# Performance work log

Hardware: AMD Instinct MI355X
Metric: run time of the kernel (lower is better)

The kernel has to match this reference:

```python
import jax, jax.numpy as jnp
import numpy as np

N, C, T, V, O, S, R = 32, 64, 256, 25, 192, 3, 8  # batch, in_ch, time, joints, out_ch, subsets, rel_ch


def setup_inputs() -> dict:
    key = jax.random.key(0)
    ks = jax.random.split(key, 20)
    w = lambda i, shape: (jax.random.normal(ks[i], shape, jnp.float32) * 0.05)
    return {
        "x": jax.random.normal(ks[0], (N, C, T, V), jnp.float32),
        "spd_A": jax.random.normal(ks[1], (V, V), jnp.float32) * 0.1,
        "A3": jax.random.normal(ks[2], (S, V, V), jnp.float32) * 0.1,
        "A6": jax.random.normal(ks[3], (6, V, V), jnp.float32) * 0.1,
        "conv1_w": w(4, (S, R, C)), "conv1_b": jnp.zeros((S, R), jnp.float32),
        "conv2_w": w(5, (S, R, C)), "conv2_b": jnp.zeros((S, R), jnp.float32),
        "conv4_w": w(6, (S, O, R)), "conv4_b": jnp.zeros((S, O), jnp.float32),
        "conv3_w": w(7, (S, O, C)), "conv3_b": jnp.zeros((S, O), jnp.float32),
        "alpha": jnp.full((1,), 0.5, jnp.float32),
        "beta": jnp.full((1,), 0.5, jnp.float32),
        "gamma": jnp.full((1,), 0.5, jnp.float32),
        "bn_w": jnp.ones((O,), jnp.float32), "bn_b": jnp.zeros((O,), jnp.float32),
        "down_w": w(8, (O, C)), "down_b": jnp.zeros((O,), jnp.float32),
        "dbn_w": jnp.ones((O,), jnp.float32), "dbn_b": jnp.zeros((O,), jnp.float32),
    }


def _bn(y, w, b):
    # BatchNorm2d in training mode: stats over (N, T, V) per channel, biased var
    mu = y.mean(axis=(0, 2, 3), keepdims=True)
    var = ((y - mu) ** 2).mean(axis=(0, 2, 3), keepdims=True)
    return (y - mu) * jax.lax.rsqrt(var + 1e-5) * w[None, :, None, None] + b[None, :, None, None]


def reference(x, spd_A, A3, A6, conv1_w, conv1_b, conv2_w, conv2_b, conv4_w, conv4_b,
              conv3_w, conv3_b, alpha, beta, gamma, bn_w, bn_b, down_w, down_b, dbn_w, dbn_b):
    out_c = conv4_w.shape[1]
    # A6 expanded: (out//6, 6, V, V) -> (out, V, V); contiguous-view == tile along channel blocks
    A6_ex = jnp.tile(A6, (out_c // 6, 1, 1))  # (O, V, V)
    # 1x1 conv then temporal mean == conv on temporal mean (linear op commutes)
    xm = x.mean(axis=2)  # (N, C, V)
    x1 = jnp.einsum('ncv,src->nsrv', xm, conv1_w) + conv1_b[None, :, :, None]
    x2 = jnp.einsum('ncv,src->nsrv', xm, conv2_w) + conv2_b[None, :, :, None]
    d = jnp.tanh(x1[..., :, None] - x2[..., None, :])  # (N, S, R, V, V)
    A_dyn = jnp.einsum('nsruv,sor->nsouv', d, conv4_w) + conv4_b[None, :, :, None, None]
    A_at = (A_dyn * alpha + A3[None, :, None, :, :]
            + A6_ex[None, None] * beta + spd_A[None, None, None] * gamma)  # (N, S, O, V, V)
    # CTRGC_2: x3 = conv3(x); einsum 'ncuv,nctv->nctu', summed over subsets
    x3 = jnp.einsum('nctv,soc->nsotv', x, conv3_w) + conv3_b[None, :, :, None, None]
    y = jnp.einsum('nsouv,nsotv->notu', A_at, x3)  # (N, O, T, V)
    y = _bn(y, bn_w, bn_b)
    xd = jnp.einsum('nctv,oc->notv', x, down_w) + down_b[None, :, None, None]
    y = jax.nn.relu(y + _bn(xd, dbn_w, dbn_b))
    return y
```

## Files before the change

kernel.cpp:

```cpp
#include <hip/hip_runtime.h>

#define N_ 32
#define C_ 64
#define T_ 256
#define V_ 25
#define O_ 192
#define S_ 3
#define R_ 8
#define VV (V_*V_)
#define TV (T_*V_)
#define RP 26
#define TRP (T_*RP)

typedef unsigned short u16;
typedef unsigned int u32;
typedef __attribute__((ext_vector_type(4))) u16 u16x4;
typedef __attribute__((ext_vector_type(8))) u16 u16x8;
typedef __attribute__((ext_vector_type(4))) u32 u32x4;
typedef __attribute__((ext_vector_type(8))) __bf16 bf16x8;
typedef __attribute__((ext_vector_type(4))) float f32x4;

#define WS_A2F_U 0
#define WS_XQ_U  (18874368)
#define WS_XD_U  (18874368 + 13631488)
#define WS_YB_U  (18874368 + 13631488 + 39321600)
#define WS_XM_F   (55574528)
#define WS_RS_F   (55574528 + 51200)
#define WS_STAT_F (55574528 + 51200 + 153600)

__device__ __forceinline__ u16 f2b(float f) {
    return __builtin_bit_cast(u16, (__bf16)f);
}
__device__ __forceinline__ float b2f(u16 u) {
    return __builtin_bit_cast(float, ((unsigned)u) << 16);
}
__device__ __forceinline__ f32x4 mfma16(bf16x8 a, bf16x8 b, f32x4 c) {
    return __builtin_amdgcn_mfma_f32_16x16x32_bf16(a, b, c, 0, 0, 0);
}
__device__ __forceinline__ float fast_tanh(float x) {
    return 1.f - 2.f * __builtin_amdgcn_rcpf(__expf(2.f * x) + 1.f);
}

__global__ void k0_xq(const float* __restrict__ x, u16* __restrict__ xq) {
    __shared__ float tile[64][52];
    int bid = blockIdx.x;
    int n = bid >> 7, tb = bid & 127;
    int t0 = tb * 2;
    int tid = threadIdx.x;
    const float2* xp = (const float2*)(x + (size_t)n * C_ * TV + t0 * 25);
    for (int p = tid; p < 1600; p += 256) {
        int c = p / 25, q = p % 25;
        float2 f2 = xp[(size_t)c * 3200 + q];
        tile[c][q * 2] = f2.x;
        tile[c][q * 2 + 1] = f2.y;
    }
    __syncthreads();
    for (int p = tid; p < 832; p += 256) {
        int row = p >> 4, c4g = p & 15;
        int t = row >= RP, v = row - t * RP;
        u16x4 w;
        #pragma unroll
        for (int i = 0; i < 4; ++i) {
            int co = ((c4g & 3) << 4) + ((c4g >> 2) << 2) + i;
            w[i] = (v < 25) ? f2b(tile[co][t * 25 + v]) : (u16)0;
        }
        *(u16x4*)&xq[((size_t)n * TRP + tb * 52 + row) * 64 + c4g * 4] = w;
    }
}

__global__ void k1_xm(const u16* __restrict__ xq, float* __restrict__ xm_out) {
    __shared__ float ps[256];
    int bid = blockIdx.x;
    int n = bid / 25, v = bid % 25;
    int tid = threadIdx.x;
    int cg = tid & 63, tg = tid >> 6;
    const u16* p = xq + (size_t)n * TRP * 64 + ((size_t)(tg * 64 * RP + v)) * 64 + cg;
    float s = 0.f;
    for (int t = 0; t < 64; ++t) {
        s += b2f(*p);
        p += RP * 64;
    }
    ps[tid] = s;
    __syncthreads();
    if (tid < 64) {
        float tot = ps[tid] + ps[64 + tid] + ps[128 + tid] + ps[192 + tid];
        int c4g = tid >> 2, i = tid & 3;
        int co = ((c4g & 3) << 4) + ((c4g >> 2) << 2) + i;
        xm_out[((size_t)n * C_ + co) * V_ + v] = tot * (1.f / T_);
    }
}

__global__ void k2_a2f(const float* __restrict__ spd, const float* __restrict__ A3,
                       const float* __restrict__ A6,
                       const float* __restrict__ w1, const float* __restrict__ b1,
                       const float* __restrict__ w2, const float* __restrict__ b2,
                       const float* __restrict__ w4, const float* __restrict__ b4,
                       const float* __restrict__ b3,
                       const float* __restrict__ alpha, const float* __restrict__ beta,
                       const float* __restrict__ gamma,
                       u16* __restrict__ a2f, const float* __restrict__ xmbuf,
                       float* __restrict__ rs_tot) {
    __shared__ float xm[C_ * V_];
    __shared__ float x1s[R_ * V_], x2s[R_ * V_];
    __shared__ float dm[R_ * VV];
    __shared__ float a3s[VV], sps[VV];
    __shared__ float aatw[4][2 * VV];
    int bid = blockIdx.x;
    int n = bid / 24;
    int rem = bid % 24;
    int s = rem / 8, og = rem % 8;
    int tid = threadIdx.x, wid = tid >> 6, lane = tid & 63;
    const float* xmg = xmbuf + (size_t)n * C_ * V_;
    for (int p = tid; p < C_ * V_; p += 256) xm[p] = xmg[p];
    for (int p = tid; p < VV; p += 256) { a3s[p] = A3[s * VV + p]; sps[p] = spd[p]; }
    __syncthreads();
    if (tid < R_ * V_) {
        int r = tid / V_, v = tid % V_;
        float acc1 = b1[s * R_ + r], acc2 = b2[s * R_ + r];
        for (int c = 0; c < C_; ++c) {
            float xv = xm[c * V_ + v];
            acc1 += xv * w1[(s * R_ + r) * C_ + c];
            acc2 += xv * w2[(s * R_ + r) * C_ + c];
        }
        x1s[tid] = acc1; x2s[tid] = acc2;
    }
    __syncthreads();
    for (int p = tid; p < R_ * VV; p += 256) {
        int r = p / VV, uv = p % VV, u = uv / V_, v = uv % V_;
        dm[p] = fast_tanh(x1s[r * V_ + u] - x2s[r * V_ + v]);
    }
    __syncthreads();
    float al = alpha[0], be = beta[0], ga = gamma[0];
    float* aat = aatw[wid];
    for (int opi = 0; opi < 3; ++opi) {
        int op = wid * 3 + opi;
        int o0 = og * 24 + op * 2;
        float w4v[2][R_], b4v[2];
        #pragma unroll
        for (int oo = 0; oo < 2; ++oo) {
            b4v[oo] = b4[s * O_ + o0 + oo];
            #pragma unroll
            for (int r = 0; r < R_; ++r)
                w4v[oo][r] = w4[((size_t)(s * O_ + o0 + oo)) * R_ + r];
        }
        const float* a6p0 = A6 + ((o0 % 6) * VV);
        for (int p = lane; p < 2 * VV; p += 64) {
            int oo = p / VV, pp = p - oo * VV;
            float acc = b4v[oo];
            #pragma unroll
            for (int r = 0; r < R_; ++r) acc += dm[r * VV + pp] * w4v[oo][r];
            aat[p] = al * acc + a3s[pp] + ga * sps[pp] + be * a6p0[oo * VV + pp];
        }
        if (lane < 2 * V_) {
            int oo = lane / V_, u = lane - oo * V_;
            float rs = 0.f;
            for (int v = 0; v < V_; ++v) rs += aat[oo * VV + u * V_ + v];
            atomicAdd(&rs_tot[((size_t)(n * O_ + o0 + oo)) * V_ + u],
                      b3[s * O_ + o0 + oo] * rs);
        }
        #pragma unroll
        for (int it = 0; it < 4; ++it) {
            int idx = it * 64 + lane;
            int oo = idx >> 7, l2 = idx & 127, cu = l2 >> 6, l = l2 & 63;
            int u = cu * 16 + (l & 15);
            u16x8 w;
            #pragma unroll
            for (int j = 0; j < 8; ++j) {
                int v = ((j >> 2) << 4) + ((l >> 4) << 2) + (j & 3);
                float val = 0.f;
                if (u < V_ && v < V_) val = aat[oo * VV + u * V_ + v];
                w[j] = f2b(val);
            }
            size_t idxg = ((((size_t)(n * O_ + o0 + oo)) * S_ + s) * 2 + cu) * 64 + l;
            ((u16x8*)a2f)[idxg] = w;
        }
    }
}

#define OSTR_B 2504
#define SSTR_B 832
#define BUF_B  20064

__global__ __launch_bounds__(256, 3)
void k3_main(const u16* __restrict__ xq,
             const float* __restrict__ w3, const float* __restrict__ dw,
             const float* __restrict__ db,
             const u16* __restrict__ a2f, const float* __restrict__ rs_tot,
             u16* __restrict__ yb16, u16* __restrict__ xdws,
             float* __restrict__ stats) {
    __shared__ char x3Lb[2 * BUF_B];
    __shared__ u16 xdst[8 * 416];
    __shared__ u16 ystage[8 * 400];
    int orig = blockIdx.x;
    int bid = (orig & 7) * 96 + (orig >> 3);
    int n = bid / 24;
    int o0 = (bid % 24) * 8;
    int tid = threadIdx.x, wid = tid >> 6, lane = tid & 63;
    int lr = lane & 15, lg = lane >> 4;
    int colt = wid & 1;
    int rt0 = (wid >> 1) * 13;

    for (int p = tid; p < 2 * BUF_B / 16; p += 256) ((u32x4*)x3Lb)[p] = u32x4{0,0,0,0};

    const float* wsrc = (colt == 0)
        ? w3 + ((size_t)((lr >> 3) * O_ + o0 + (lr & 7))) * C_
        : ((lr < 8) ? w3 + ((size_t)(2 * O_ + o0 + lr)) * C_
                    : dw + ((size_t)(o0 + lr - 8)) * C_);
    bf16x8 bw[2];
    #pragma unroll
    for (int ks = 0; ks < 2; ++ks) {
        u16x8 tmp;
        #pragma unroll
        for (int j = 0; j < 8; ++j) {
            int c = ks * 32 + (lg << 2) + (j & 3) + ((j >> 2) << 4);
            tmp[j] = f2b(wsrc[c]);
        }
        bw[ks] = __builtin_bit_cast(bf16x8, tmp);
    }
    float dbv = (colt == 1 && lr >= 8) ? db[o0 + lr - 8] : 0.f;

    int wo = (colt == 0) ? (lr & 7) : lr;
    int wsb = (colt == 0) ? (lr >> 3) : 2;
    int colbyte = wo * OSTR_B + wsb * SSTR_B;

    const bf16x8* a2v = (const bf16x8*)a2f;
    bf16x8 Bh[2][6];
    float rsb0[2], rsb1[2];
    #pragma unroll
    for (int oi = 0; oi < 2; ++oi) {
        int o = o0 + (wid << 1) + oi;
        const bf16x8* bp = a2v + ((size_t)(n * O_ + o)) * 6 * 64 + lane;
        #pragma unroll
        for (int q = 0; q < 6; ++q) Bh[oi][q] = bp[(size_t)q * 64];
        const float* rsp = rs_tot + ((size_t)(n * O_ + o)) * V_;
        rsb0[oi] = rsp[lr];
        rsb1[oi] = (lr < 9) ? rsp[16 + lr] : 0.f;
    }

    float sy1[2] = {0, 0}, sy2[2] = {0, 0};
    float sd1 = 0.f, sd2 = 0.f;
    const u16* xbn = xq + (size_t)n * TRP * 64;
    int rdw = 13 * lr + 2 * lg;
    char* buf = x3Lb;
    int t0 = 0;

    auto tl = [&](int ch, int j, u16x8& A0, u16x8& A1) {
        const u16* p = xbn + ((size_t)(ch * 16) * RP + (size_t)((rt0 + j) * 16 + lr)) * 64
                       + (lg << 4);
        A0 = *(const u16x8*)p;
        A1 = *(const u16x8*)(p + 8);
    };
    auto proc = [&](int rt, u16x8 A0, u16x8 A1) {
        f32x4 acc = {0.f, 0.f, 0.f, 0.f};
        acc = mfma16(__builtin_bit_cast(bf16x8, A0), bw[0], acc);
        acc = mfma16(__builtin_bit_cast(bf16x8, A1), bw[1], acc);
        int rbase = rt * 16 + (lg << 2);
        if (colt == 0 || lr < 8) {
            u16x4 w;
            #pragma unroll
            for (int reg = 0; reg < 4; ++reg) w[reg] = f2b(acc[reg]);
            *(u16x4*)(buf + colbyte + rbase * 2) = w;
        } else {
            u16x4 w;
            #pragma unroll
            for (int reg = 0; reg < 4; ++reg) {
                int rr = rbase + reg;
                int t = rr / RP, v = rr - t * RP;
                float val = acc[reg] + dbv;
                w[reg] = f2b(val);
                if (v < 25) { sd1 += val; sd2 += val * val; }
            }
            *(u16x4*)&xdst[(lr - 8) * 416 + rbase] = w;
        }
    };

    __syncthreads();

    u16x8 p0a, p0b, p1a, p1b, p2a, p2b, p3a, p3b;
    tl(0, 0, p0a, p0b); tl(0, 1, p1a, p1b); tl(0, 2, p2a, p2b); tl(0, 3, p3a, p3b);

    for (int ch = 0; ch < 16; ++ch) {
        t0 = ch * 16;
        buf = x3Lb + (ch & 1) * BUF_B;
        proc(rt0 + 0, p0a, p0b);
        proc(rt0 + 1, p1a, p1b);
        proc(rt0 + 2, p2a, p2b);
        proc(rt0 + 3, p3a, p3b);
        for (int j = 4; j < 13; ++j) {
            u16x8 A0, A1;
            tl(ch, j, A0, A1);
            proc(rt0 + j, A0, A1);
        }
        if (ch < 15) {
            tl(ch + 1, 0, p0a, p0b); tl(ch + 1, 1, p1a, p1b);
            tl(ch + 1, 2, p2a, p2b); tl(ch + 1, 3, p3a, p3b);
        }
        __syncthreads();
        #pragma unroll
        for (int oi = 0; oi < 2; ++oi) {
            int ol = (wid << 1) + oi;
            const u32* L = (const u32*)(buf + ol * OSTR_B);
            f32x4 acc0 = {0, 0, 0, 0}, acc1 = {0, 0, 0, 0};
            #pragma unroll
            for (int s = 0; s < 3; ++s) {
                const u32* Ls = L + s * 208 + rdw;
                u32 d0 = Ls[0], d1 = Ls[1], d8 = Ls[8], d9 = Ls[9];
                bf16x8 A = __builtin_bit_cast(bf16x8, u32x4{d0, d1, d8, d9});
                acc0 = mfma16(A, Bh[oi][s * 2 + 0], acc0);
                acc1 = mfma16(A, Bh[oi][s * 2 + 1], acc1);
            }
            int ylb = ol * 400 + (lg << 2) * 25;
            #pragma unroll
            for (int reg = 0; reg < 4; ++reg) {
                float v0 = acc0[reg] + rsb0[oi];
                ystage[ylb + reg * 25 + lr] = f2b(v0);
                sy1[oi] += v0; sy2[oi] += v0 * v0;
                if (lr < 9) {
                    float v1 = acc1[reg] + rsb1[oi];
                    ystage[ylb + reg * 25 + 16 + lr] = f2b(v1);
                    sy1[oi] += v1; sy2[oi] += v1 * v1;
                }
            }
        }
        {
            size_t ygb = (size_t)(n * O_ + o0) * TV + (size_t)t0 * V_;
            for (int q = lane; q < 100; q += 64) {
                int sel = q >= 50;
                int ol2 = (wid << 1) + sel;
                int j = q - sel * 50;
                u16x8 pk = *(const u16x8*)&ystage[ol2 * 400 + j * 8];
                *(u16x8*)&yb16[ygb + (size_t)ol2 * TV + j * 8] = pk;
            }
        }
        if (colt == 1) {
            int tofs = (wid >> 1) * 8;
            size_t gdb = (size_t)(n * O_ + o0) * TV + (size_t)(t0 + tofs) * V_;
            for (int q = lane; q < 200; q += 64) {
                int o = q / 25, w = q - o * 25;
                int g0 = w * 8;
                int tl2 = g0 / 25, v = g0 - tl2 * 25;
                u16x8 pk;
                #pragma unroll
                for (int k = 0; k < 8; ++k) {
                    pk[k] = xdst[o * 416 + (tofs + tl2) * RP + v];
                    if (++v == 25) { v = 0; ++tl2; }
                }
                *(u16x8*)&xdws[gdb + (size_t)o * TV + g0] = pk;
            }
        }
    }
    #pragma unroll
    for (int oi = 0; oi < 2; ++oi) {
        float v1 = sy1[oi], v2 = sy2[oi];
        #pragma unroll
        for (int m = 1; m < 64; m <<= 1) {
            v1 += __shfl_xor(v1, m);
            v2 += __shfl_xor(v2, m);
        }
        if (lane == 0) {
            atomicAdd(&stats[0 * O_ + o0 + (wid << 1) + oi], v1);
            atomicAdd(&stats[1 * O_ + o0 + (wid << 1) + oi], v2);
        }
    }
    if (colt == 1) {
        float v1 = sd1, v2 = sd2;
        v1 += __shfl_xor(v1, 16); v2 += __shfl_xor(v2, 16);
        v1 += __shfl_xor(v1, 32); v2 += __shfl_xor(v2, 32);
        if (lane >= 8 && lane < 16) {
            atomicAdd(&stats[2 * O_ + o0 + lane - 8], v1);
            atomicAdd(&stats[3 * O_ + o0 + lane - 8], v2);
        }
    }
}

__global__ void k5_final(float* __restrict__ out, const u16* __restrict__ yb,
                         const u16* __restrict__ xd, const float* __restrict__ stats,
                         const float* __restrict__ bn_w, const float* __restrict__ bn_b,
                         const float* __restrict__ dbn_w, const float* __restrict__ dbn_b) {
    __shared__ float cf[4 * O_];
    int tid = threadIdx.x;
    if (tid < O_) {
        int o = tid;
        float inv = 1.f / (float)(N_ * T_ * V_);
        float mu_y = stats[o] * inv;
        float var_y = stats[O_ + o] * inv - mu_y * mu_y;
        float ay = bn_w[o] * rsqrtf(var_y + 1e-5f);
        float by = bn_b[o] - mu_y * ay;
        float mu_d = stats[2 * O_ + o] * inv;
        float var_d = stats[3 * O_ + o] * inv - mu_d * mu_d;
        float ad = dbn_w[o] * rsqrtf(var_d + 1e-5f);
        float bd = dbn_b[o] - mu_d * ad;
        cf[o] = ay; cf[O_ + o] = by; cf[2 * O_ + o] = ad; cf[3 * O_ + o] = bd;
    }
    __syncthreads();
    size_t total = (size_t)N_ * O_ * TV / 8;
    for (size_t i = blockIdx.x * (size_t)blockDim.x + tid; i < total;
         i += (size_t)gridDim.x * blockDim.x) {
        int o = (int)((i / 800) % O_);
        float ay = cf[o], by = cf[O_ + o], ad = cf[2 * O_ + o], bd = cf[3 * O_ + o];
        u16x8 yv = ((const u16x8*)yb)[i];
        u16x8 dv = ((const u16x8*)xd)[i];
        float4 r0, r1;
        r0.x = fmaxf(ay * b2f(yv[0]) + by + ad * b2f(dv[0]) + bd, 0.f);
        r0.y = fmaxf(ay * b2f(yv[1]) + by + ad * b2f(dv[1]) + bd, 0.f);
        r0.z = fmaxf(ay * b2f(yv[2]) + by + ad * b2f(dv[2]) + bd, 0.f);
        r0.w = fmaxf(ay * b2f(yv[3]) + by + ad * b2f(dv[3]) + bd, 0.f);
        r1.x = fmaxf(ay * b2f(yv[4]) + by + ad * b2f(dv[4]) + bd, 0.f);
        r1.y = fmaxf(ay * b2f(yv[5]) + by + ad * b2f(dv[5]) + bd, 0.f);
        r1.z = fmaxf(ay * b2f(yv[6]) + by + ad * b2f(dv[6]) + bd, 0.f);
        r1.w = fmaxf(ay * b2f(yv[7]) + by + ad * b2f(dv[7]) + bd, 0.f);
        ((float4*)out)[2 * i] = r0;
        ((float4*)out)[2 * i + 1] = r1;
    }
}

extern "C" void kernel_launch(void* const* d_in, const int* in_sizes, int n_in,
                              void* d_out, int out_size, void* d_ws, size_t ws_size,
                              hipStream_t stream) {
    const float* x     = (const float*)d_in[0];
    const float* spd   = (const float*)d_in[1];
    const float* A3    = (const float*)d_in[2];
    const float* A6    = (const float*)d_in[3];
    const float* w1    = (const float*)d_in[4];
    const float* b1    = (const float*)d_in[5];
    const float* w2    = (const float*)d_in[6];
    const float* b2    = (const float*)d_in[7];
    const float* w4    = (const float*)d_in[8];
    const float* b4    = (const float*)d_in[9];
    const float* w3    = (const float*)d_in[10];
    const float* b3    = (const float*)d_in[11];
    const float* alpha = (const float*)d_in[12];
    const float* beta  = (const float*)d_in[13];
    const float* gamma = (const float*)d_in[14];
    const float* bn_w  = (const float*)d_in[15];
    const float* bn_b  = (const float*)d_in[16];
    const float* dw    = (const float*)d_in[17];
    const float* db    = (const float*)d_in[18];
    const float* dbn_w = (const float*)d_in[19];
    const float* dbn_b = (const float*)d_in[20];
    float* out = (float*)d_out;
    u16*   wsu = (u16*)d_ws;
    float* wsf = (float*)d_ws;

    u16* a2f  = wsu + WS_A2F_U;
    u16* xq   = wsu + WS_XQ_U;
    u16* xd   = wsu + WS_XD_U;
    u16* yb   = wsu + WS_YB_U;
    float* xm    = wsf + WS_XM_F;
    float* rs    = wsf + WS_RS_F;
    float* stats = wsf + WS_STAT_F;

    hipMemsetAsync(rs, 0, (N_ * O_ * V_ + 4 * O_) * sizeof(float), stream);

    k0_xq<<<N_ * 128, 256, 0, stream>>>(x, xq);
    k1_xm<<<N_ * 25, 256, 0, stream>>>(xq, xm);
    k2_a2f<<<N_ * S_ * 8, 256, 0, stream>>>(spd, A3, A6, w1, b1, w2, b2, w4, b4, b3,
                                            alpha, beta, gamma, a2f, xm, rs);
    k3_main<<<N_ * 24, 256, 0, stream>>>(xq, w3, dw, db, a2f, rs, yb, xd, stats);
    k5_final<<<4096, 256, 0, stream>>>(out, yb, xd, stats, bn_w, bn_b, dbn_w, dbn_b);
}
```

Before: 308.7 us.

## Double k3_main block to 512 threads, one output channel per wave

k3_main now launches 512 threads (8 waves) per block instead of 256. Each wave handles one output channel rather than two, and the 26 row tiles of the x3 conv are split 7/7/6/6 across the four wave pairs. The register prefetch pipeline of the next chunk's inputs is removed and replaced by straightforward loads. A second barrier per chunk is added, and every wave now writes its own xd rows. The intent is more parallelism and latency hiding per block, at the cost of lost software prefetch and extra synchronisation.

```diff
diff --git a/kernel.cpp b/kernel.cpp
--- a/kernel.cpp
+++ b/kernel.cpp
@@ -181,7 +181,7 @@
 #define SSTR_B 832
 #define BUF_B  20064
 
-__global__ __launch_bounds__(256, 3)
+__global__ __launch_bounds__(512, 6)
 void k3_main(const u16* __restrict__ xq,
              const float* __restrict__ w3, const float* __restrict__ dw,
              const float* __restrict__ db,
@@ -198,9 +198,11 @@
     int tid = threadIdx.x, wid = tid >> 6, lane = tid & 63;
     int lr = lane & 15, lg = lane >> 4;
     int colt = wid & 1;
-    int rt0 = (wid >> 1) * 13;
-
-    for (int p = tid; p < 2 * BUF_B / 16; p += 256) ((u32x4*)x3Lb)[p] = u32x4{0,0,0,0};
+    int tq = wid >> 1;
+    int rt0 = tq * 7 - (tq == 3 ? 1 : 0);
+    int cnt = (tq < 2) ? 7 : 6;
+
+    for (int p = tid; p < 2 * BUF_B / 16; p += 512) ((u32x4*)x3Lb)[p] = u32x4{0,0,0,0};
 
     const float* wsrc = (colt == 0)
         ? w3 + ((size_t)((lr >> 3) * O_ + o0 + (lr & 7))) * C_
@@ -224,142 +226,114 @@
     int colbyte = wo * OSTR_B + wsb * SSTR_B;
 
     const bf16x8* a2v = (const bf16x8*)a2f;
-    bf16x8 Bh[2][6];
-    float rsb0[2], rsb1[2];
-    #pragma unroll
-    for (int oi = 0; oi < 2; ++oi) {
-        int o = o0 + (wid << 1) + oi;
+    bf16x8 Bh[6];
+    float rsb0, rsb1;
+    {
+        int o = o0 + wid;
         const bf16x8* bp = a2v + ((size_t)(n * O_ + o)) * 6 * 64 + lane;
         #pragma unroll
-        for (int q = 0; q < 6; ++q) Bh[oi][q] = bp[(size_t)q * 64];
+        for (int q = 0; q < 6; ++q) Bh[q] = bp[(size_t)q * 64];
         const float* rsp = rs_tot + ((size_t)(n * O_ + o)) * V_;
-        rsb0[oi] = rsp[lr];
-        rsb1[oi] = (lr < 9) ? rsp[16 + lr] : 0.f;
-    }
-
-    float sy1[2] = {0, 0}, sy2[2] = {0, 0};
+        rsb0 = rsp[lr];
+        rsb1 = (lr < 9) ? rsp[16 + lr] : 0.f;
+    }
+
+    float sy1 = 0.f, sy2 = 0.f;
     float sd1 = 0.f, sd2 = 0.f;
     const u16* xbn = xq + (size_t)n * TRP * 64;
     int rdw = 13 * lr + 2 * lg;
-    char* buf = x3Lb;
-    int t0 = 0;
-
-    auto tl = [&](int ch, int j, u16x8& A0, u16x8& A1) {
-        const u16* p = xbn + ((size_t)(ch * 16) * RP + (size_t)((rt0 + j) * 16 + lr)) * 64
-                       + (lg << 4);
-        A0 = *(const u16x8*)p;
-        A1 = *(const u16x8*)(p + 8);
-    };
-    auto proc = [&](int rt, u16x8 A0, u16x8 A1) {
-        f32x4 acc = {0.f, 0.f, 0.f, 0.f};
-        acc = mfma16(__builtin_bit_cast(bf16x8, A0), bw[0], acc);
-        acc = mfma16(__builtin_bit_cast(bf16x8, A1), bw[1], acc);
-        int rbase = rt * 16 + (lg << 2);
-        if (colt == 0 || lr < 8) {
-            u16x4 w;
-            #pragma unroll
-            for (int reg = 0; reg < 4; ++reg) w[reg] = f2b(acc[reg]);
-            *(u16x4*)(buf + colbyte + rbase * 2) = w;
-        } else {
-            u16x4 w;
-            #pragma unroll
-            for (int reg = 0; reg < 4; ++reg) {
-                int rr = rbase + reg;
-                int t = rr / RP, v = rr - t * RP;
-                float val = acc[reg] + dbv;
-                w[reg] = f2b(val);
-                if (v < 25) { sd1 += val; sd2 += val * val; }
-            }
-            *(u16x4*)&xdst[(lr - 8) * 416 + rbase] = w;
-        }
-    };
-
-    __syncthreads();
-
-    u16x8 p0a, p0b, p1a, p1b, p2a, p2b, p3a, p3b;
-    tl(0, 0, p0a, p0b); tl(0, 1, p1a, p1b); tl(0, 2, p2a, p2b); tl(0, 3, p3a, p3b);
+
+    __syncthreads();
 
     for (int ch = 0; ch < 16; ++ch) {
-        t0 = ch * 16;
-        buf = x3Lb + (ch & 1) * BUF_B;
-        proc(rt0 + 0, p0a, p0b);
-        proc(rt0 + 1, p1a, p1b);
-        proc(rt0 + 2, p2a, p2b);
-        proc(rt0 + 3, p3a, p3b);
-        for (int j = 4; j < 13; ++j) {
-            u16x8 A0, A1;
-            tl(ch, j, A0, A1);
-            proc(rt0 + j, A0, A1);
-        }
-        if (ch < 15) {
-            tl(ch + 1, 0, p0a, p0b); tl(ch + 1, 1, p1a, p1b);
-            tl(ch + 1, 2, p2a, p2b); tl(ch + 1, 3, p3a, p3b);
+        int t0 = ch * 16;
+        char* buf = x3Lb + (ch & 1) * BUF_B;
+        const u16* xrow = xbn + (size_t)t0 * RP * 64;
+        for (int j = 0; j < cnt; ++j) {
+            int rt = rt0 + j;
+            const u16* ap = xrow + (size_t)(rt * 16 + lr) * 64 + (lg << 4);
+            u16x8 A0 = *(const u16x8*)ap;
+            u16x8 A1 = *(const u16x8*)(ap + 8);
+            f32x4 acc = {0.f, 0.f, 0.f, 0.f};
+            acc = mfma16(__builtin_bit_cast(bf16x8, A0), bw[0], acc);
+            acc = mfma16(__builtin_bit_cast(bf16x8, A1), bw[1], acc);
+            int rbase = rt * 16 + (lg << 2);
+            if (colt == 0 || lr < 8) {
+                u16x4 w;
+                #pragma unroll
+                for (int reg = 0; reg < 4; ++reg) w[reg] = f2b(acc[reg]);
+                *(u16x4*)(buf + colbyte + rbase * 2) = w;
+            } else {
+                u16x4 w;
+                #pragma unroll
+                for (int reg = 0; reg < 4; ++reg) {
+                    int rr = rbase + reg;
+                    int t = rr / RP, v = rr - t * RP;
+                    float val = acc[reg] + dbv;
+                    w[reg] = f2b(val);
+                    if (v < 25) { sd1 += val; sd2 += val * val; }
+                }
+                *(u16x4*)&xdst[(lr - 8) * 416 + rbase] = w;
+            }
         }
         __syncthreads();
-        #pragma unroll
-        for (int oi = 0; oi < 2; ++oi) {
-            int ol = (wid << 1) + oi;
-            const u32* L = (const u32*)(buf + ol * OSTR_B);
+        {
+            const u32* L = (const u32*)(buf + wid * OSTR_B);
             f32x4 acc0 = {0, 0, 0, 0}, acc1 = {0, 0, 0, 0};
             #pragma unroll
             for (int s = 0; s < 3; ++s) {
                 const u32* Ls = L + s * 208 + rdw;
                 u32 d0 = Ls[0], d1 = Ls[1], d8 = Ls[8], d9 = Ls[9];
                 bf16x8 A = __builtin_bit_cast(bf16x8, u32x4{d0, d1, d8, d9});
-                acc0 = mfma16(A, Bh[oi][s * 2 + 0], acc0);
-                acc1 = mfma16(A, Bh[oi][s * 2 + 1], acc1);
-            }
-            int ylb = ol * 400 + (lg << 2) * 25;
+                acc0 = mfma16(A, Bh[s * 2 + 0], acc0);
+                acc1 = mfma16(A, Bh[s * 2 + 1], acc1);
+            }
+            int ylb = wid * 400 + (lg << 2) * 25;
             #pragma unroll
             for (int reg = 0; reg < 4; ++reg) {
-                float v0 = acc0[reg] + rsb0[oi];
+                float v0 = acc0[reg] + rsb0;
                 ystage[ylb + reg * 25 + lr] = f2b(v0);
-                sy1[oi] += v0; sy2[oi] += v0 * v0;
+                sy1 += v0; sy2 += v0 * v0;
                 if (lr < 9) {
-                    float v1 = acc1[reg] + rsb1[oi];
+                    float v1 = acc1[reg] + rsb1;
                     ystage[ylb + reg * 25 + 16 + lr] = f2b(v1);
-                    sy1[oi] += v1; sy2[oi] += v1 * v1;
+                    sy1 += v1; sy2 += v1 * v1;
                 }
             }
         }
         {
-            size_t ygb = (size_t)(n * O_ + o0) * TV + (size_t)t0 * V_;
-            for (int q = lane; q < 100; q += 64) {
-                int sel = q >= 50;
-                int ol2 = (wid << 1) + sel;
-                int j = q - sel * 50;
-                u16x8 pk = *(const u16x8*)&ystage[ol2 * 400 + j * 8];
-                *(u16x8*)&yb16[ygb + (size_t)ol2 * TV + j * 8] = pk;
-            }
-        }
-        if (colt == 1) {
-            int tofs = (wid >> 1) * 8;
-            size_t gdb = (size_t)(n * O_ + o0) * TV + (size_t)(t0 + tofs) * V_;
-            for (int q = lane; q < 200; q += 64) {
-                int o = q / 25, w = q - o * 25;
-                int g0 = w * 8;
+            size_t ygb = (size_t)(n * O_ + o0 + wid) * TV + (size_t)t0 * V_;
+            if (lane < 50) {
+                u16x8 pk = *(const u16x8*)&ystage[wid * 400 + lane * 8];
+                *(u16x8*)&yb16[ygb + lane * 8] = pk;
+            }
+        }
+        {
+            size_t gdb = (size_t)(n * O_ + o0 + wid) * TV + (size_t)t0 * V_;
+            if (lane < 50) {
+                int g0 = lane * 8;
                 int tl2 = g0 / 25, v = g0 - tl2 * 25;
                 u16x8 pk;
                 #pragma unroll
                 for (int k = 0; k < 8; ++k) {
-                    pk[k] = xdst[o * 416 + (tofs + tl2) * RP + v];
+                    pk[k] = xdst[wid * 416 + tl2 * RP + v];
                     if (++v == 25) { v = 0; ++tl2; }
                 }
-                *(u16x8*)&xdws[gdb + (size_t)o * TV + g0] = pk;
-            }
-        }
-    }
-    #pragma unroll
-    for (int oi = 0; oi < 2; ++oi) {
-        float v1 = sy1[oi], v2 = sy2[oi];
+                *(u16x8*)&xdws[gdb + g0] = pk;
+            }
+        }
+        __syncthreads();
+    }
+    {
+        float v1 = sy1, v2 = sy2;
         #pragma unroll
         for (int m = 1; m < 64; m <<= 1) {
             v1 += __shfl_xor(v1, m);
             v2 += __shfl_xor(v2, m);
         }
         if (lane == 0) {
-            atomicAdd(&stats[0 * O_ + o0 + (wid << 1) + oi], v1);
-            atomicAdd(&stats[1 * O_ + o0 + (wid << 1) + oi], v2);
+            atomicAdd(&stats[0 * O_ + o0 + wid], v1);
+            atomicAdd(&stats[1 * O_ + o0 + wid], v2);
         }
     }
     if (colt == 1) {
@@ -456,6 +430,6 @@
     k1_xm<<<N_ * 25, 256, 0, stream>>>(xq, xm);
     k2_a2f<<<N_ * S_ * 8, 256, 0, stream>>>(spd, A3, A6, w1, b1, w2, b2, w4, b4, b3,
                                             alpha, beta, gamma, a2f, xm, rs);
-    k3_main<<<N_ * 24, 256, 0, stream>>>(xq, w3, dw, db, a2f, rs, yb, xd, stats);
+    k3_main<<<N_ * 24, 512, 0, stream>>>(xq, w3, dw, db, a2f, rs, yb, xd, stats);
     k5_final<<<4096, 256, 0, stream>>>(out, yb, xd, stats, bn_w, bn_b, dbn_w, dbn_b);
 }
```

After: 302.3 us. -2.1%, faster.
